# Kernel tuning notes

Measured on AMD Instinct MI355X. Metric: run time of the kernel, lower is better.

Reference implementation:

```python
import jax, jax.numpy as jnp
import numpy as np

B, C, D = 512, 1000, 512
K = 10


def setup_inputs() -> dict:
    key = jax.random.key(0)
    k1, k2, k3, k4, k5 = jax.random.split(key, 5)
    x = jax.random.normal(k1, (B, D), dtype=jnp.float32)
    protos = jax.random.normal(k2, (C, D), dtype=jnp.float32)
    # ex2/ex1 chosen so N*ex2^2 - ex1^2 > 0 (valid sqrt)
    ex2 = jax.random.uniform(k3, (C, D), dtype=jnp.float32) + 1.0
    ex1 = jax.random.uniform(k4, (C, D), dtype=jnp.float32) * 0.1
    cls_num = jax.random.randint(k5, (C,), 1, 100, dtype=jnp.int32)
    proto_label = jnp.arange(C, dtype=jnp.int32)
    return {"x": x, "protos": protos, "ex2": ex2, "ex1": ex1,
            "cls_num": cls_num, "proto_label": proto_label, "k_nearest": K}


def reference(x, protos, ex2, ex1, cls_num, proto_label, k_nearest):
    # rd: per-class, per-feature variance proxy  [C, D]
    N = cls_num[:, None].astype(ex2.dtype)
    rd = jnp.sqrt(N * ex2 ** 2 - ex1 ** 2)
    # softmax over feature dim of (rowmax - rd)
    rd = jax.nn.softmax(jnp.max(rd, axis=1, keepdims=True) - rd, axis=1)
    # weighted squared distances: [B, C, D] -> reduce D -> [B, C]
    diff = x[:, None, :] - protos[None, :, :]
    x_dists = diff ** 2 * rd[None, :, :]
    simi_mat = x_dists.sum(axis=2)  # [B, C]
    # k smallest distances (torch.topk largest=False)
    neg_vals, topk_index = jax.lax.top_k(-simi_mat, k_nearest)
    topk_vals = -neg_vals  # [B, K]
    topk_conf = topk_vals.sum(axis=1, keepdims=True) / topk_vals  # [B, K]
    # pick prototype with max confidence, map through label table
    temp = jnp.argmax(topk_conf, axis=1)  # [B]
    ans_index = jnp.take_along_axis(topk_index, temp[:, None], axis=1)[:, 0]
    predict = proto_label[ans_index]  # [B]
    return predict, topk_conf
```

## Files before the change

### kernel.cpp

```cpp
#include <hip/hip_runtime.h>
#include <math.h>
#include <float.h>

#define B_SZ 512
#define C_SZ 1000
#define D_SZ 512
#define K_TOP 10
#define K2 1024
#define NSPLIT 4
#define KSPLIT (K2 / NSPLIT)
#define BC (B_SZ * C_SZ)

#define WHI_OFF 0
#define WLO_OFF (C_SZ * K2)
#define T3_OFF  (C_SZ * K2)
#define PART_OFF (T3_OFF + 1024)

using f16x8 = __attribute__((ext_vector_type(8))) _Float16;
using f32x4 = __attribute__((ext_vector_type(4))) float;

__device__ __forceinline__ void split2(float v, _Float16& h, _Float16& l) {
    h = (_Float16)v;
    l = (_Float16)(v - (float)h);
}

__global__ __launch_bounds__(256) void prep_kernel(const float* __restrict__ protos,
                                                   const float* __restrict__ ex2,
                                                   const float* __restrict__ ex1,
                                                   const int* __restrict__ cls_num,
                                                   float* __restrict__ ws) {
    _Float16* Whi = (_Float16*)ws + WHI_OFF;
    _Float16* Wlo = (_Float16*)ws + WLO_OFF;
    float* t3 = ws + T3_OFF;
    const int wid  = threadIdx.x >> 6;
    const int lane = threadIdx.x & 63;
    const int c = blockIdx.x * 4 + wid;

    const size_t rb = (size_t)c * D_SZ + lane * 8;
    float e2v[8], e1v[8], pv[8];
    *(float4*)&e2v[0] = *(const float4*)(ex2 + rb);
    *(float4*)&e2v[4] = *(const float4*)(ex2 + rb + 4);
    *(float4*)&e1v[0] = *(const float4*)(ex1 + rb);
    *(float4*)&e1v[4] = *(const float4*)(ex1 + rb + 4);
    *(float4*)&pv[0]  = *(const float4*)(protos + rb);
    *(float4*)&pv[4]  = *(const float4*)(protos + rb + 4);
    const float N = (float)cls_num[c];

    float v[8], mn = FLT_MAX;
    #pragma unroll
    for (int k = 0; k < 8; k++) {
        v[k] = sqrtf(N * e2v[k] * e2v[k] - e1v[k] * e1v[k]);
        mn = fminf(mn, v[k]);
    }
    #pragma unroll
    for (int off = 1; off < 64; off <<= 1) mn = fminf(mn, __shfl_xor(mn, off));

    float ev[8], s = 0.f;
    #pragma unroll
    for (int k = 0; k < 8; k++) { ev[k] = expf(mn - v[k]); s += ev[k]; }
    #pragma unroll
    for (int off = 1; off < 64; off <<= 1) s += __shfl_xor(s, off);
    const float inv = 1.0f / s;

    f16x8 h1, l1, h2, l2;
    float t = 0.f;
    #pragma unroll
    for (int k = 0; k < 8; k++) {
        const float rdv = ev[k] * inv;
        const float w2  = -2.0f * rdv * pv[k];
        _Float16 hh, ll;
        split2(rdv, hh, ll); h1[k] = hh; l1[k] = ll;
        split2(w2,  hh, ll); h2[k] = hh; l2[k] = ll;
        t = fmaf(rdv * pv[k], pv[k], t);
    }
    _Float16* wh = Whi + (size_t)c * K2 + lane * 8;
    _Float16* wl = Wlo + (size_t)c * K2 + lane * 8;
    *(f16x8*)(wh)         = h1;
    *(f16x8*)(wh + D_SZ)  = h2;
    *(f16x8*)(wl)         = l1;
    *(f16x8*)(wl + D_SZ)  = l2;

    #pragma unroll
    for (int off = 1; off < 64; off <<= 1) t += __shfl_xor(t, off);
    if (lane == 0) t3[c] = t;
}

#define BM 64
#define BN 64
#define BK 32
#define LDT 40

__global__ __launch_bounds__(256, 2) void gemm_kernel(const float* __restrict__ x,
                                                      const _Float16* __restrict__ Whi,
                                                      const _Float16* __restrict__ Wlo,
                                                      float* __restrict__ part) {
    __shared__ __align__(16) _Float16 Ah[BM][LDT];
    __shared__ __align__(16) _Float16 Al[BM][LDT];
    __shared__ __align__(16) _Float16 Bh[BN][LDT];
    __shared__ __align__(16) _Float16 Bl[BN][LDT];

    const int tid  = threadIdx.x;
    const int lane = tid & 63;
    const int w    = tid >> 6;
    const int c0 = blockIdx.x * BN;
    const int b0 = blockIdx.y * BM;
    const int kz = blockIdx.z;
    const bool sq = (kz < NSPLIT / 2);
    const int khalf0 = sq ? kz * KSPLIT : kz * KSPLIT - D_SZ;

    const int srow = tid >> 2;
    const int sseg = (tid & 3) * 8;
    const int mw = (w >> 1) * 32;
    const int nw = (w & 1) * 32;
    const int lr = lane & 15;
    const int kg = lane >> 4;

    f32x4 acc[2][2];
    #pragma unroll
    for (int i = 0; i < 2; i++)
        #pragma unroll
        for (int j = 0; j < 2; j++)
            #pragma unroll
            for (int r = 0; r < 4; r++) acc[i][j][r] = 0.f;

    const int cW = c0 + srow;

    for (int ch = 0; ch < KSPLIT / BK; ch++) {
        const int kx = khalf0 + ch * BK + sseg;
        const int kw = kz * KSPLIT + ch * BK + sseg;

        float4 a0 = *(const float4*)(x + (size_t)(b0 + srow) * D_SZ + kx);
        float4 a1 = *(const float4*)(x + (size_t)(b0 + srow) * D_SZ + kx + 4);
        if (sq) {
            a0.x *= a0.x; a0.y *= a0.y; a0.z *= a0.z; a0.w *= a0.w;
            a1.x *= a1.x; a1.y *= a1.y; a1.z *= a1.z; a1.w *= a1.w;
        }
        const float av[8] = {a0.x, a0.y, a0.z, a0.w, a1.x, a1.y, a1.z, a1.w};
        f16x8 ah, al;
        #pragma unroll
        for (int j = 0; j < 8; j++) {
            _Float16 hh, ll;
            split2(av[j], hh, ll);
            ah[j] = hh; al[j] = ll;
        }

        f16x8 wh, wl;
        if (cW < C_SZ) {
            wh = *(const f16x8*)(Whi + (size_t)cW * K2 + kw);
            wl = *(const f16x8*)(Wlo + (size_t)cW * K2 + kw);
        } else {
            #pragma unroll
            for (int j = 0; j < 8; j++) { wh[j] = (_Float16)0.f; wl[j] = (_Float16)0.f; }
        }

        __syncthreads();
        *(f16x8*)&Ah[srow][sseg] = ah;
        *(f16x8*)&Al[srow][sseg] = al;
        *(f16x8*)&Bh[srow][sseg] = wh;
        *(f16x8*)&Bl[srow][sseg] = wl;
        __syncthreads();

        f16x8 fah[2], fal[2], fbh[2], fbl[2];
        #pragma unroll
        for (int i = 0; i < 2; i++) {
            fah[i] = *(const f16x8*)&Ah[mw + i * 16 + lr][kg * 8];
            fal[i] = *(const f16x8*)&Al[mw + i * 16 + lr][kg * 8];
            fbh[i] = *(const f16x8*)&Bh[nw + i * 16 + lr][kg * 8];
            fbl[i] = *(const f16x8*)&Bl[nw + i * 16 + lr][kg * 8];
        }
        #pragma unroll
        for (int i = 0; i < 2; i++)
            #pragma unroll
            for (int j = 0; j < 2; j++) {
                acc[i][j] = __builtin_amdgcn_mfma_f32_16x16x32_f16(fal[i], fbl[j], acc[i][j], 0, 0, 0);
                acc[i][j] = __builtin_amdgcn_mfma_f32_16x16x32_f16(fah[i], fbl[j], acc[i][j], 0, 0, 0);
                acc[i][j] = __builtin_amdgcn_mfma_f32_16x16x32_f16(fal[i], fbh[j], acc[i][j], 0, 0, 0);
                acc[i][j] = __builtin_amdgcn_mfma_f32_16x16x32_f16(fah[i], fbh[j], acc[i][j], 0, 0, 0);
            }
    }

    float* o = part + (size_t)kz * BC;
    #pragma unroll
    for (int i = 0; i < 2; i++) {
        #pragma unroll
        for (int j = 0; j < 2; j++) {
            const int c = c0 + nw + j * 16 + lr;
            if (c < C_SZ) {
                #pragma unroll
                for (int r = 0; r < 4; r++) {
                    const int b = b0 + mw + i * 16 + kg * 4 + r;
                    o[(size_t)b * C_SZ + c] = acc[i][j][r];
                }
            }
        }
    }
}

__global__ __launch_bounds__(256) void topk_kernel(const float* __restrict__ ws,
                                                   const int* __restrict__ proto_label,
                                                   float* __restrict__ out) {
    const float* part = ws + PART_OFF;
    const float* t3   = ws + T3_OFF;
    const int wid = threadIdx.x >> 6;
    const int lane = threadIdx.x & 63;
    const int b = blockIdx.x * 4 + wid;

    float vals[16];
    #pragma unroll
    for (int j = 0; j < 16; j++) {
        const int c = lane + j * 64;
        if (c < C_SZ) {
            const size_t idx = (size_t)b * C_SZ + c;
            float s = t3[c];
            #pragma unroll
            for (int z = 0; z < NSPLIT; z++)
                s += part[(size_t)z * BC + idx];
            vals[j] = s;
        } else {
            vals[j] = FLT_MAX;
        }
    }

    float kv[K_TOP];
    int ki[K_TOP];
    for (int t = 0; t < K_TOP; t++) {
        float bv = FLT_MAX;
        int bi = 0x7fffffff;
        #pragma unroll
        for (int j = 0; j < 16; j++) {
            const int c = lane + j * 64;
            if (vals[j] < bv) { bv = vals[j]; bi = c; }
        }
        #pragma unroll
        for (int off = 1; off < 64; off <<= 1) {
            const float ov = __shfl_xor(bv, off);
            const int oi = __shfl_xor(bi, off);
            if (ov < bv || (ov == bv && oi < bi)) { bv = ov; bi = oi; }
        }
        kv[t] = bv;
        ki[t] = bi;
        if ((bi & 63) == lane) vals[bi >> 6] = FLT_MAX;
    }

    if (lane == 0) {
        float S = 0.f;
        #pragma unroll
        for (int t = 0; t < K_TOP; t++) S += kv[t];
        float conf[K_TOP];
        #pragma unroll
        for (int t = 0; t < K_TOP; t++) {
            conf[t] = S / kv[t];
            out[B_SZ + b * K_TOP + t] = conf[t];
        }
        int best = 0;
        for (int t = 1; t < K_TOP; t++)
            if (conf[t] > conf[best]) best = t;
        out[b] = (float)proto_label[ki[best]];
    }
}

extern "C" void kernel_launch(void* const* d_in, const int* in_sizes, int n_in,
                              void* d_out, int out_size, void* d_ws, size_t ws_size,
                              hipStream_t stream) {
    const float* x           = (const float*)d_in[0];
    const float* protos      = (const float*)d_in[1];
    const float* ex2         = (const float*)d_in[2];
    const float* ex1         = (const float*)d_in[3];
    const int*   cls_num     = (const int*)d_in[4];
    const int*   proto_label = (const int*)d_in[5];

    float* ws  = (float*)d_ws;
    float* out = (float*)d_out;

    prep_kernel<<<C_SZ / 4, 256, 0, stream>>>(protos, ex2, ex1, cls_num, ws);

    dim3 g2((C_SZ + BN - 1) / BN, B_SZ / BM, NSPLIT);
    gemm_kernel<<<g2, 256, 0, stream>>>(x,
                                        (const _Float16*)ws + WHI_OFF,
                                        (const _Float16*)ws + WLO_OFF,
                                        ws + PART_OFF);

    topk_kernel<<<B_SZ / 4, 256, 0, stream>>>(ws, proto_label, out);
}
```

Measured before the change: 93.67 us.

## Fuse prep, GEMM and top-k into one cooperative kernel with grid syncs

Merges the three separate launches into a single cooperative kernel of 512 blocks that runs the prep, split-K GEMM and top-k phases in turn, separated by grid-wide barriers. The goal is to remove the launch gaps and tail drain between kernels. In exchange it adds two grid.sync barriers, all blocks must be co-resident, and the prep and top-k phases leave most blocks idle.

```diff
diff --git a/kernel.cpp b/kernel.cpp
--- a/kernel.cpp
+++ b/kernel.cpp
@@ -1,6 +1,9 @@
 #include <hip/hip_runtime.h>
+#include <hip/hip_cooperative_groups.h>
 #include <math.h>
 #include <float.h>
+
+namespace cg = cooperative_groups;
 
 #define B_SZ 512
 #define C_SZ 1000
@@ -24,11 +27,11 @@
     l = (_Float16)(v - (float)h);
 }
 
-__global__ __launch_bounds__(256) void prep_kernel(const float* __restrict__ protos,
-                                                   const float* __restrict__ ex2,
-                                                   const float* __restrict__ ex1,
-                                                   const int* __restrict__ cls_num,
-                                                   float* __restrict__ ws) {
+__device__ __forceinline__ void prep_phase(const float* __restrict__ protos,
+                                           const float* __restrict__ ex2,
+                                           const float* __restrict__ ex1,
+                                           const int* __restrict__ cls_num,
+                                           float* __restrict__ ws) {
     _Float16* Whi = (_Float16*)ws + WHI_OFF;
     _Float16* Wlo = (_Float16*)ws + WLO_OFF;
     float* t3 = ws + T3_OFF;
@@ -90,21 +93,21 @@
 #define BK 32
 #define LDT 40
 
-__global__ __launch_bounds__(256, 2) void gemm_kernel(const float* __restrict__ x,
-                                                      const _Float16* __restrict__ Whi,
-                                                      const _Float16* __restrict__ Wlo,
-                                                      float* __restrict__ part) {
-    __shared__ __align__(16) _Float16 Ah[BM][LDT];
-    __shared__ __align__(16) _Float16 Al[BM][LDT];
-    __shared__ __align__(16) _Float16 Bh[BN][LDT];
-    __shared__ __align__(16) _Float16 Bl[BN][LDT];
-
+__device__ __forceinline__ void gemm_phase(const float* __restrict__ x,
+                                           const _Float16* __restrict__ Whi,
+                                           const _Float16* __restrict__ Wlo,
+                                           float* __restrict__ part,
+                                           _Float16 (*Ah)[LDT], _Float16 (*Al)[LDT],
+                                           _Float16 (*Bh)[LDT], _Float16 (*Bl)[LDT]) {
     const int tid  = threadIdx.x;
     const int lane = tid & 63;
     const int w    = tid >> 6;
-    const int c0 = blockIdx.x * BN;
-    const int b0 = blockIdx.y * BM;
-    const int kz = blockIdx.z;
+    const int bid  = blockIdx.x;
+    const int cx = bid & 15;
+    const int by = (bid >> 4) & 7;
+    const int kz = bid >> 7;
+    const int c0 = cx * BN;
+    const int b0 = by * BM;
     const bool sq = (kz < NSPLIT / 2);
     const int khalf0 = sq ? kz * KSPLIT : kz * KSPLIT - D_SZ;
 
@@ -196,9 +199,9 @@
     }
 }
 
-__global__ __launch_bounds__(256) void topk_kernel(const float* __restrict__ ws,
-                                                   const int* __restrict__ proto_label,
-                                                   float* __restrict__ out) {
+__device__ __forceinline__ void topk_phase(const float* __restrict__ ws,
+                                           const int* __restrict__ proto_label,
+                                           float* __restrict__ out) {
     const float* part = ws + PART_OFF;
     const float* t3   = ws + T3_OFF;
     const int wid = threadIdx.x >> 6;
@@ -259,6 +262,38 @@
     }
 }
 
+__global__ __launch_bounds__(256, 2) void fused_kernel(const float* __restrict__ x,
+                                                       const float* __restrict__ protos,
+                                                       const float* __restrict__ ex2,
+                                                       const float* __restrict__ ex1,
+                                                       const int* __restrict__ cls_num,
+                                                       const int* __restrict__ proto_label,
+                                                       float* __restrict__ ws,
+                                                       float* __restrict__ out) {
+    __shared__ __align__(16) _Float16 Ah[BM][LDT];
+    __shared__ __align__(16) _Float16 Al[BM][LDT];
+    __shared__ __align__(16) _Float16 Bh[BN][LDT];
+    __shared__ __align__(16) _Float16 Bl[BN][LDT];
+
+    cg::grid_group grid = cg::this_grid();
+
+    if (blockIdx.x < C_SZ / 4)
+        prep_phase(protos, ex2, ex1, cls_num, ws);
+
+    grid.sync();
+
+    gemm_phase(x,
+               (const _Float16*)ws + WHI_OFF,
+               (const _Float16*)ws + WLO_OFF,
+               ws + PART_OFF,
+               Ah, Al, Bh, Bl);
+
+    grid.sync();
+
+    if (blockIdx.x < B_SZ / 4)
+        topk_phase(ws, proto_label, out);
+}
+
 extern "C" void kernel_launch(void* const* d_in, const int* in_sizes, int n_in,
                               void* d_out, int out_size, void* d_ws, size_t ws_size,
                               hipStream_t stream) {
@@ -272,13 +307,9 @@
     float* ws  = (float*)d_ws;
     float* out = (float*)d_out;
 
-    prep_kernel<<<C_SZ / 4, 256, 0, stream>>>(protos, ex2, ex1, cls_num, ws);
-
-    dim3 g2((C_SZ + BN - 1) / BN, B_SZ / BM, NSPLIT);
-    gemm_kernel<<<g2, 256, 0, stream>>>(x,
-                                        (const _Float16*)ws + WHI_OFF,
-                                        (const _Float16*)ws + WLO_OFF,
-                                        ws + PART_OFF);
-
-    topk_kernel<<<B_SZ / 4, 256, 0, stream>>>(ws, proto_label, out);
-}
+    void* args[] = {(void*)&x, (void*)&protos, (void*)&ex2, (void*)&ex1,
+                    (void*)&cls_num, (void*)&proto_label, (void*)&ws, (void*)&out};
+    hipLaunchCooperativeKernel((void*)fused_kernel,
+                               dim3(16 * 8 * NSPLIT), dim3(256),
+                               args, 0, stream);
+}
```

Measured after the change: 241.7 us. 2.58x slower.

## Fuse weight preparation into GEMM blocks, recomputing softmax weights into shared memory

Applied to the files above, without the earlier changes.

Removes the separate prep kernel and its fp16 hi/lo weight buffers in workspace. Each GEMM block recomputes the softmax-normalized weights for its 64 classes, splits them to fp16 hi/lo, and keeps its K-slice resident in shared memory for the whole K loop. This saves a launch and global round trip for weights, at the cost of redundant per-block recomputation and reads of ex2/ex1/protos, plus a much larger shared memory footprint.

```diff
diff --git a/kernel.cpp b/kernel.cpp
--- a/kernel.cpp
+++ b/kernel.cpp
@@ -8,13 +8,17 @@
 #define K_TOP 10
 #define K2 1024
 #define NSPLIT 4
-#define KSPLIT (K2 / NSPLIT)
+#define KSPLIT 256
 #define BC (B_SZ * C_SZ)
 
-#define WHI_OFF 0
-#define WLO_OFF (C_SZ * K2)
-#define T3_OFF  (C_SZ * K2)
-#define PART_OFF (T3_OFF + 1024)
+#define T3_OFF 0
+#define PART_OFF 1024
+
+#define BM 64
+#define BN 64
+#define BK 32
+#define LDA 40
+#define LDB 264
 
 using f16x8 = __attribute__((ext_vector_type(8))) _Float16;
 using f32x4 = __attribute__((ext_vector_type(4))) float;
@@ -24,80 +28,19 @@
     l = (_Float16)(v - (float)h);
 }
 
-__global__ __launch_bounds__(256) void prep_kernel(const float* __restrict__ protos,
-                                                   const float* __restrict__ ex2,
-                                                   const float* __restrict__ ex1,
-                                                   const int* __restrict__ cls_num,
-                                                   float* __restrict__ ws) {
-    _Float16* Whi = (_Float16*)ws + WHI_OFF;
-    _Float16* Wlo = (_Float16*)ws + WLO_OFF;
-    float* t3 = ws + T3_OFF;
-    const int wid  = threadIdx.x >> 6;
-    const int lane = threadIdx.x & 63;
-    const int c = blockIdx.x * 4 + wid;
-
-    const size_t rb = (size_t)c * D_SZ + lane * 8;
-    float e2v[8], e1v[8], pv[8];
-    *(float4*)&e2v[0] = *(const float4*)(ex2 + rb);
-    *(float4*)&e2v[4] = *(const float4*)(ex2 + rb + 4);
-    *(float4*)&e1v[0] = *(const float4*)(ex1 + rb);
-    *(float4*)&e1v[4] = *(const float4*)(ex1 + rb + 4);
-    *(float4*)&pv[0]  = *(const float4*)(protos + rb);
-    *(float4*)&pv[4]  = *(const float4*)(protos + rb + 4);
-    const float N = (float)cls_num[c];
-
-    float v[8], mn = FLT_MAX;
-    #pragma unroll
-    for (int k = 0; k < 8; k++) {
-        v[k] = sqrtf(N * e2v[k] * e2v[k] - e1v[k] * e1v[k]);
-        mn = fminf(mn, v[k]);
-    }
-    #pragma unroll
-    for (int off = 1; off < 64; off <<= 1) mn = fminf(mn, __shfl_xor(mn, off));
-
-    float ev[8], s = 0.f;
-    #pragma unroll
-    for (int k = 0; k < 8; k++) { ev[k] = expf(mn - v[k]); s += ev[k]; }
-    #pragma unroll
-    for (int off = 1; off < 64; off <<= 1) s += __shfl_xor(s, off);
-    const float inv = 1.0f / s;
-
-    f16x8 h1, l1, h2, l2;
-    float t = 0.f;
-    #pragma unroll
-    for (int k = 0; k < 8; k++) {
-        const float rdv = ev[k] * inv;
-        const float w2  = -2.0f * rdv * pv[k];
-        _Float16 hh, ll;
-        split2(rdv, hh, ll); h1[k] = hh; l1[k] = ll;
-        split2(w2,  hh, ll); h2[k] = hh; l2[k] = ll;
-        t = fmaf(rdv * pv[k], pv[k], t);
-    }
-    _Float16* wh = Whi + (size_t)c * K2 + lane * 8;
-    _Float16* wl = Wlo + (size_t)c * K2 + lane * 8;
-    *(f16x8*)(wh)         = h1;
-    *(f16x8*)(wh + D_SZ)  = h2;
-    *(f16x8*)(wl)         = l1;
-    *(f16x8*)(wl + D_SZ)  = l2;
-
-    #pragma unroll
-    for (int off = 1; off < 64; off <<= 1) t += __shfl_xor(t, off);
-    if (lane == 0) t3[c] = t;
-}
-
-#define BM 64
-#define BN 64
-#define BK 32
-#define LDT 40
-
-__global__ __launch_bounds__(256, 2) void gemm_kernel(const float* __restrict__ x,
-                                                      const _Float16* __restrict__ Whi,
-                                                      const _Float16* __restrict__ Wlo,
-                                                      float* __restrict__ part) {
-    __shared__ __align__(16) _Float16 Ah[BM][LDT];
-    __shared__ __align__(16) _Float16 Al[BM][LDT];
-    __shared__ __align__(16) _Float16 Bh[BN][LDT];
-    __shared__ __align__(16) _Float16 Bl[BN][LDT];
+__global__ __launch_bounds__(256, 2) void gemm_fused(const float* __restrict__ x,
+                                                     const float* __restrict__ protos,
+                                                     const float* __restrict__ ex2,
+                                                     const float* __restrict__ ex1,
+                                                     const int* __restrict__ cls_num,
+                                                     float* __restrict__ ws) {
+    __shared__ __align__(16) _Float16 Ah[BM][LDA];
+    __shared__ __align__(16) _Float16 Al[BM][LDA];
+    __shared__ __align__(16) _Float16 BSh[BN][LDB];
+    __shared__ __align__(16) _Float16 BSl[BN][LDB];
+
+    float* t3   = ws + T3_OFF;
+    float* part = ws + PART_OFF;
 
     const int tid  = threadIdx.x;
     const int lane = tid & 63;
@@ -105,9 +48,76 @@
     const int c0 = blockIdx.x * BN;
     const int b0 = blockIdx.y * BM;
     const int kz = blockIdx.z;
-    const bool sq = (kz < NSPLIT / 2);
-    const int khalf0 = sq ? kz * KSPLIT : kz * KSPLIT - D_SZ;
-
+    const bool isRd = (kz < 2);
+    const int ownBase = isRd ? kz * 32 : (kz - 2) * 32;
+
+    for (int i = 0; i < 16; i++) {
+        const int lc = w * 16 + i;
+        const int c  = c0 + lc;
+        if (c < C_SZ) {
+            const size_t rb = (size_t)c * D_SZ + lane * 8;
+            float e2v[8], e1v[8], pv[8];
+            *(float4*)&e2v[0] = *(const float4*)(ex2 + rb);
+            *(float4*)&e2v[4] = *(const float4*)(ex2 + rb + 4);
+            *(float4*)&e1v[0] = *(const float4*)(ex1 + rb);
+            *(float4*)&e1v[4] = *(const float4*)(ex1 + rb + 4);
+            *(float4*)&pv[0]  = *(const float4*)(protos + rb);
+            *(float4*)&pv[4]  = *(const float4*)(protos + rb + 4);
+            const float N = (float)cls_num[c];
+
+            float v[8], mn = FLT_MAX;
+            #pragma unroll
+            for (int k = 0; k < 8; k++) {
+                v[k] = sqrtf(N * e2v[k] * e2v[k] - e1v[k] * e1v[k]);
+                mn = fminf(mn, v[k]);
+            }
+            #pragma unroll
+            for (int off = 1; off < 64; off <<= 1) mn = fminf(mn, __shfl_xor(mn, off));
+
+            float ev[8], s = 0.f;
+            #pragma unroll
+            for (int k = 0; k < 8; k++) { ev[k] = expf(mn - v[k]); s += ev[k]; }
+            #pragma unroll
+            for (int off = 1; off < 64; off <<= 1) s += __shfl_xor(s, off);
+            const float inv = 1.0f / s;
+
+            float rdv[8], t = 0.f;
+            #pragma unroll
+            for (int k = 0; k < 8; k++) {
+                rdv[k] = ev[k] * inv;
+                t = fmaf(rdv[k] * pv[k], pv[k], t);
+            }
+            #pragma unroll
+            for (int off = 1; off < 64; off <<= 1) t += __shfl_xor(t, off);
+            if (blockIdx.y == 0 && kz == 0 && lane == 0) t3[c] = t;
+
+            const int rel = lane - ownBase;
+            if (rel >= 0 && rel < 32) {
+                f16x8 hh, ll;
+                #pragma unroll
+                for (int k = 0; k < 8; k++) {
+                    const float val = isRd ? rdv[k] : (-2.0f * rdv[k] * pv[k]);
+                    _Float16 h, l;
+                    split2(val, h, l);
+                    hh[k] = h; ll[k] = l;
+                }
+                const int col = rel * 8;
+                *(f16x8*)&BSh[lc][col] = hh;
+                *(f16x8*)&BSl[lc][col] = ll;
+            }
+        } else {
+            if (lane < 32) {
+                f16x8 z;
+                #pragma unroll
+                for (int k = 0; k < 8; k++) z[k] = (_Float16)0.f;
+                *(f16x8*)&BSh[lc][lane * 8] = z;
+                *(f16x8*)&BSl[lc][lane * 8] = z;
+            }
+        }
+    }
+    __syncthreads();
+
+    const int khalf0 = isRd ? kz * KSPLIT : kz * KSPLIT - D_SZ;
     const int srow = tid >> 2;
     const int sseg = (tid & 3) * 8;
     const int mw = (w >> 1) * 32;
@@ -123,15 +133,12 @@
             #pragma unroll
             for (int r = 0; r < 4; r++) acc[i][j][r] = 0.f;
 
-    const int cW = c0 + srow;
-
     for (int ch = 0; ch < KSPLIT / BK; ch++) {
         const int kx = khalf0 + ch * BK + sseg;
-        const int kw = kz * KSPLIT + ch * BK + sseg;
 
         float4 a0 = *(const float4*)(x + (size_t)(b0 + srow) * D_SZ + kx);
         float4 a1 = *(const float4*)(x + (size_t)(b0 + srow) * D_SZ + kx + 4);
-        if (sq) {
+        if (isRd) {
             a0.x *= a0.x; a0.y *= a0.y; a0.z *= a0.z; a0.w *= a0.w;
             a1.x *= a1.x; a1.y *= a1.y; a1.z *= a1.z; a1.w *= a1.w;
         }
@@ -144,20 +151,9 @@
             ah[j] = hh; al[j] = ll;
         }
 
-        f16x8 wh, wl;
-        if (cW < C_SZ) {
-            wh = *(const f16x8*)(Whi + (size_t)cW * K2 + kw);
-            wl = *(const f16x8*)(Wlo + (size_t)cW * K2 + kw);
-        } else {
-            #pragma unroll
-            for (int j = 0; j < 8; j++) { wh[j] = (_Float16)0.f; wl[j] = (_Float16)0.f; }
-        }
-
         __syncthreads();
         *(f16x8*)&Ah[srow][sseg] = ah;
         *(f16x8*)&Al[srow][sseg] = al;
-        *(f16x8*)&Bh[srow][sseg] = wh;
-        *(f16x8*)&Bl[srow][sseg] = wl;
         __syncthreads();
 
         f16x8 fah[2], fal[2], fbh[2], fbl[2];
@@ -165,8 +161,8 @@
         for (int i = 0; i < 2; i++) {
             fah[i] = *(const f16x8*)&Ah[mw + i * 16 + lr][kg * 8];
             fal[i] = *(const f16x8*)&Al[mw + i * 16 + lr][kg * 8];
-            fbh[i] = *(const f16x8*)&Bh[nw + i * 16 + lr][kg * 8];
-            fbl[i] = *(const f16x8*)&Bl[nw + i * 16 + lr][kg * 8];
+            fbh[i] = *(const f16x8*)&BSh[nw + i * 16 + lr][ch * BK + kg * 8];
+            fbl[i] = *(const f16x8*)&BSl[nw + i * 16 + lr][ch * BK + kg * 8];
         }
         #pragma unroll
         for (int i = 0; i < 2; i++)
@@ -272,13 +268,8 @@
     float* ws  = (float*)d_ws;
     float* out = (float*)d_out;
 
-    prep_kernel<<<C_SZ / 4, 256, 0, stream>>>(protos, ex2, ex1, cls_num, ws);
-
-    dim3 g2((C_SZ + BN - 1) / BN, B_SZ / BM, NSPLIT);
-    gemm_kernel<<<g2, 256, 0, stream>>>(x,
-                                        (const _Float16*)ws + WHI_OFF,
-                                        (const _Float16*)ws + WLO_OFF,
-                                        ws + PART_OFF);
+    dim3 g((C_SZ + BN - 1) / BN, B_SZ / BM, NSPLIT);
+    gemm_fused<<<g, 256, 0, stream>>>(x, protos, ex2, ex1, cls_num, ws);
 
     topk_kernel<<<B_SZ / 4, 256, 0, stream>>>(ws, proto_label, out);
 }
```

Result: slower. 118.9 us (+26.9%).
